# Kernel tuning notes

Measured on AMD Instinct MI355X. Metric: run time of the kernel, lower is better.

Reference implementation:

```python
import jax, jax.numpy as jnp
import numpy as np

B, H, W, C = 16, 56, 56, 512
WS, NH = 7, 16
HD = C // NH
HID = 4 * C
N = WS * WS
NW = (H // WS) * (W // WS)
SCALE = HD ** -0.5
EPS = 1e-5


def _layernorm(x, g, b):
    mu = jnp.mean(x, axis=-1, keepdims=True)
    var = jnp.mean(jnp.square(x - mu), axis=-1, keepdims=True)
    return (x - mu) * jax.lax.rsqrt(var + EPS) * g + b


def _win_part(t):
    # (B,H,W,C) -> (B*nw, NH, N, HD)
    t = t.reshape(B, H // WS, WS, W // WS, WS, C).transpose(0, 1, 3, 2, 4, 5)
    return t.reshape(B * NW, N, NH, HD).transpose(0, 2, 1, 3)


def setup_inputs() -> dict:
    key = jax.random.key(0)
    ks = jax.random.split(key, 20)
    p = lambda k, shp: (jax.random.normal(k, shp, dtype=jnp.float32) * 0.02)
    return {
        "x": jax.random.normal(ks[0], (B, H * W, C), dtype=jnp.float32),
        "Wq": p(ks[1], (C, C)), "bq": jnp.zeros((C,), jnp.float32),
        "Wk": p(ks[2], (C, C)), "bk": jnp.zeros((C,), jnp.float32),
        "Wv": p(ks[3], (C, C)), "bv": jnp.zeros((C,), jnp.float32),
        "Wp": p(ks[4], (C, C)), "bp": jnp.zeros((C,), jnp.float32),
        "rel_bias": p(ks[5], (1, NH, N, N)),
        "g1": jnp.ones((C,), jnp.float32), "b1": jnp.zeros((C,), jnp.float32),
        "g2": jnp.ones((C,), jnp.float32), "b2": jnp.zeros((C,), jnp.float32),
        "W1": p(ks[6], (C, HID)), "bfc1": jnp.zeros((HID,), jnp.float32),
        "W2": p(ks[7], (HID, C)), "bfc2": jnp.zeros((C,), jnp.float32),
    }


def reference(x, Wq, bq, Wk, bk, Wv, bv, Wp, bp, rel_bias,
              g1, b1, g2, b2, W1, bfc1, W2, bfc2):
    shortcut = x                                   # (B, L, C)
    h = _layernorm(x, g1, b1).reshape(B, H, W, C)
    q = _win_part(h @ Wq + bq)                     # (B*nw, NH, N, HD)
    k = _win_part(h @ Wk + bk)
    v = _win_part(h @ Wv + bv)
    attn = jnp.einsum("whnd,whmd->whnm", q * SCALE, k) + rel_bias
    attn = jax.nn.softmax(attn, axis=-1)
    out = jnp.einsum("whnm,whmd->whnd", attn, v)   # (B*nw, NH, N, HD)
    out = out.transpose(0, 2, 1, 3).reshape(B * NW, N, C)
    out = out @ Wp + bp
    # window reverse -> (B, L, C)
    out = out.reshape(B, H // WS, W // WS, WS, WS, C)
    out = out.transpose(0, 1, 3, 2, 4, 5).reshape(B, H * W, C)
    x = shortcut + out
    h2 = _layernorm(x, g2, b2)
    h2 = jax.nn.gelu(h2 @ W1 + bfc1, approximate=False) @ W2 + bfc2
    return x + h2
```

## Files before the change

### kernel.cpp

```cpp
#include <hip/hip_runtime.h>

typedef unsigned short u16;
typedef unsigned int   u32;

using short8  = __attribute__((ext_vector_type(8))) short;
using floatx4 = __attribute__((ext_vector_type(4))) float;

#define Bb   16
#define Hh   56
#define Ww   56
#define Cc   512
#define NHh  16
#define HDd  32
#define HIDh 2048
#define Ll   (Hh*Ww)
#define Mm   (Bb*Ll)
#define SCALE 0.17677669529663687f
#define CSTR 136
#define PSTR 72

__device__ __forceinline__ u16 f2bf(float f) {
  union { float f; u32 u; } v; v.f = f;
  u32 r = (v.u + 0x7fffu + ((v.u >> 16) & 1u)) >> 16;
  return (u16)r;
}
__device__ __forceinline__ float bf2f(u16 u) {
  union { u32 u; float f; } v; v.u = ((u32)u) << 16; return v.f;
}
__device__ __forceinline__ float bf2f_lo(u32 u) {
  union { u32 u; float f; } v; v.u = u << 16; return v.f;
}
__device__ __forceinline__ float bf2f_hi(u32 u) {
  union { u32 u; float f; } v; v.u = u & 0xffff0000u; return v.f;
}
__device__ __forceinline__ float gelu_f(float x) {
  const float z  = x * 0.70710678118654752f;
  const float az = fabsf(z);
  const float t  = __builtin_amdgcn_rcpf(fmaf(0.3275911f, az, 1.f));
  float p = fmaf(1.061405429f, t, -1.453152027f);
  p = fmaf(p, t, 1.421413741f);
  p = fmaf(p, t, -0.284496736f);
  p = fmaf(p, t, 0.254829592f);
  const float e = p * t * __expf(-z * z);
  float erfz = 1.f - e;
  erfz = copysignf(erfz, z);
  return 0.5f * x * (1.f + erfz);
}
__device__ __forceinline__ void gld_lds16(const u16* g, u16* l) {
  __builtin_amdgcn_global_load_lds(
      (__attribute__((address_space(1))) void*)(void*)g,
      (__attribute__((address_space(3))) void*)(void*)l,
      16, 0, 0);
}

__global__ void wcvt_k(const float* __restrict__ W, u16* __restrict__ Wt,
                       int K, int N) {
  int idx = blockIdx.x * 256 + threadIdx.x;
  int n = idx / K;
  int k = idx - n * K;
  Wt[idx] = f2bf(W[(size_t)k * N + n]);
}

__global__ void bcat_k(const float* __restrict__ a, const float* __restrict__ b,
                       const float* __restrict__ c, float* __restrict__ o) {
  int i = blockIdx.x * 256 + threadIdx.x;
  float v = (i < 512) ? a[i] : (i < 1024) ? b[i - 512] : c[i - 1024];
  o[i] = v;
}

__global__ void relprep_k(const float* __restrict__ rel, float* __restrict__ relL) {
  int idx  = blockIdx.x * 256 + threadIdx.x;
  int reg  = idx & 3;
  int lane = (idx >> 2) & 63;
  int frag = (idx >> 8) & 15;
  int h    = idx >> 12;
  int mi = frag >> 2, nj = frag & 3;
  int row = mi * 16 + (lane >> 4) * 4 + reg;
  int col = nj * 16 + (lane & 15);
  float v;
  if (col >= 49)      v = -1e30f;
  else if (row >= 49) v = 0.f;
  else                v = rel[((size_t)h * 49 + row) * 49 + col];
  relL[idx] = v;
}

__global__ __launch_bounds__(256)
void ln_k(const float* __restrict__ x, const float* __restrict__ g,
          const float* __restrict__ b, u16* __restrict__ out) {
  const int row  = blockIdx.x * 4 + (threadIdx.x >> 6);
  const int lane = threadIdx.x & 63;
  const float* xr = x + (size_t)row * Cc + lane * 8;
  float4 v0 = *(const float4*)xr;
  float4 v1 = *(const float4*)(xr + 4);
  float s  = v0.x+v0.y+v0.z+v0.w + v1.x+v1.y+v1.z+v1.w;
  float s2 = v0.x*v0.x+v0.y*v0.y+v0.z*v0.z+v0.w*v0.w
           + v1.x*v1.x+v1.y*v1.y+v1.z*v1.z+v1.w*v1.w;
  #pragma unroll
  for (int off = 32; off >= 1; off >>= 1) {
    s  += __shfl_xor(s,  off);
    s2 += __shfl_xor(s2, off);
  }
  float mu  = s  * (1.f/512.f);
  float var = s2 * (1.f/512.f) - mu*mu;
  float rs  = rsqrtf(var + 1e-5f);
  float4 ga = *(const float4*)(g + lane*8);
  float4 gb = *(const float4*)(g + lane*8 + 4);
  float4 ba = *(const float4*)(b + lane*8);
  float4 bb = *(const float4*)(b + lane*8 + 4);
  float o0 = (v0.x-mu)*rs*ga.x + ba.x;
  float o1 = (v0.y-mu)*rs*ga.y + ba.y;
  float o2 = (v0.z-mu)*rs*ga.z + ba.z;
  float o3 = (v0.w-mu)*rs*ga.w + ba.w;
  float o4 = (v1.x-mu)*rs*gb.x + bb.x;
  float o5 = (v1.y-mu)*rs*gb.y + bb.y;
  float o6 = (v1.z-mu)*rs*gb.z + bb.z;
  float o7 = (v1.w-mu)*rs*gb.w + bb.w;
  u32 w0 = (u32)f2bf(o0) | ((u32)f2bf(o1) << 16);
  u32 w1 = (u32)f2bf(o2) | ((u32)f2bf(o3) << 16);
  u32 w2 = (u32)f2bf(o4) | ((u32)f2bf(o5) << 16);
  u32 w3 = (u32)f2bf(o6) | ((u32)f2bf(o7) << 16);
  *(uint4*)(out + (size_t)row * Cc + lane * 8) = make_uint4(w0, w1, w2, w3);
}

__global__ __launch_bounds__(256)
void ln_bf_k(const u16* __restrict__ x, const float* __restrict__ g,
             const float* __restrict__ b, u16* __restrict__ out) {
  const int row  = blockIdx.x * 4 + (threadIdx.x >> 6);
  const int lane = threadIdx.x & 63;
  uint4 xv = *(const uint4*)(x + (size_t)row * Cc + lane * 8);
  float v[8];
  v[0]=bf2f_lo(xv.x); v[1]=bf2f_hi(xv.x); v[2]=bf2f_lo(xv.y); v[3]=bf2f_hi(xv.y);
  v[4]=bf2f_lo(xv.z); v[5]=bf2f_hi(xv.z); v[6]=bf2f_lo(xv.w); v[7]=bf2f_hi(xv.w);
  float s = 0.f, s2 = 0.f;
  #pragma unroll
  for (int i = 0; i < 8; i++) { s += v[i]; s2 += v[i]*v[i]; }
  #pragma unroll
  for (int off = 32; off >= 1; off >>= 1) {
    s  += __shfl_xor(s,  off);
    s2 += __shfl_xor(s2, off);
  }
  float mu  = s  * (1.f/512.f);
  float var = s2 * (1.f/512.f) - mu*mu;
  float rs  = rsqrtf(var + 1e-5f);
  float4 ga = *(const float4*)(g + lane*8);
  float4 gb = *(const float4*)(g + lane*8 + 4);
  float4 ba = *(const float4*)(b + lane*8);
  float4 bb = *(const float4*)(b + lane*8 + 4);
  float o[8];
  o[0]=(v[0]-mu)*rs*ga.x+ba.x; o[1]=(v[1]-mu)*rs*ga.y+ba.y;
  o[2]=(v[2]-mu)*rs*ga.z+ba.z; o[3]=(v[3]-mu)*rs*ga.w+ba.w;
  o[4]=(v[4]-mu)*rs*gb.x+bb.x; o[5]=(v[5]-mu)*rs*gb.y+bb.y;
  o[6]=(v[6]-mu)*rs*gb.z+bb.z; o[7]=(v[7]-mu)*rs*gb.w+bb.w;
  u32 w0 = (u32)f2bf(o[0]) | ((u32)f2bf(o[1]) << 16);
  u32 w1 = (u32)f2bf(o[2]) | ((u32)f2bf(o[3]) << 16);
  u32 w2 = (u32)f2bf(o[4]) | ((u32)f2bf(o[5]) << 16);
  u32 w3 = (u32)f2bf(o[6]) | ((u32)f2bf(o[7]) << 16);
  *(uint4*)(out + (size_t)row * Cc + lane * 8) = make_uint4(w0, w1, w2, w3);
}

template<int MODE>
__global__ __launch_bounds__(256, 4)
void gemm_bt(const u16* __restrict__ A, const u16* __restrict__ Bt,
             const float* __restrict__ bias, const void* __restrict__ res,
             void* __restrict__ outp, int M, int N, int K, int nbn) {
  (void)M;
  __shared__ __align__(16) u16 smem[128 * CSTR];

  const int b   = blockIdx.x;
  const int xcd = b & 7;
  const int s   = b >> 3;
  const int mt  = (s / nbn) * 8 + xcd;
  const int nt  = s - (s / nbn) * nbn;
  const int m0  = mt * 128;
  const int n0  = nt * 128;

  const int tid  = threadIdx.x;
  const int lane = tid & 63;
  const int wave = tid >> 6;
  const int wm = (wave >> 1) * 64;
  const int wn = (wave & 1) * 64;
  const int quad = lane >> 4;
  const int l16  = lane & 15;

  floatx4 acc[4][4];
  #pragma unroll
  for (int i = 0; i < 4; i++)
    #pragma unroll
    for (int j = 0; j < 4; j++) acc[i][j] = (floatx4)0.f;

  const int r0  = tid >> 2;
  const int cc0 = (((tid & 3) ^ ((r0 >> 1) & 3)) * 8);
  const u16* Ag = A  + (size_t)m0 * K;
  const u16* Bg = Bt + (size_t)n0 * K;

  const int fswz = (l16 >> 1) & 3;
  const int aoff = (quad ^ fswz) * 8;

#define STG(kk, bufo) do {                                                        \
    gld_lds16(Ag + (size_t)r0        * K + (kk) + cc0, &smem[(bufo) + wave * 512]);        \
    gld_lds16(Ag + (size_t)(r0 + 64) * K + (kk) + cc0, &smem[(bufo) + 2048 + wave * 512]); \
    gld_lds16(Bg + (size_t)r0        * K + (kk) + cc0, &smem[(bufo) + 4096 + wave * 512]); \
    gld_lds16(Bg + (size_t)(r0 + 64) * K + (kk) + cc0, &smem[(bufo) + 6144 + wave * 512]); \
  } while (0)

  STG(0, 0);
  asm volatile("s_waitcnt vmcnt(0)" ::: "memory");
  __builtin_amdgcn_s_barrier();

  for (int k0 = 0; k0 < K; k0 += 32) {
    const int bufo = ((k0 >> 5) & 1) * 8192;
    if (k0 + 32 < K) STG(k0 + 32, bufo ^ 8192);
    const u16* As = &smem[bufo];
    const u16* Bs = &smem[bufo + 4096];
    short8 af[4], bf[4];
    #pragma unroll
    for (int mi = 0; mi < 4; mi++)
      af[mi] = *(const short8*)&As[(wm + mi*16 + l16) * 32 + aoff];
    #pragma unroll
    for (int ni = 0; ni < 4; ni++)
      bf[ni] = *(const short8*)&Bs[(wn + ni*16 + l16) * 32 + aoff];
    #pragma unroll
    for (int mi = 0; mi < 4; mi++)
      #pragma unroll
      for (int ni = 0; ni < 4; ni++)
        acc[mi][ni] = __builtin_amdgcn_mfma_f32_16x16x32_bf16(
            af[mi], bf[ni], acc[mi][ni], 0, 0, 0);
    asm volatile("s_waitcnt vmcnt(0)" ::: "memory");
    __builtin_amdgcn_s_barrier();
  }
#undef STG

  if (MODE == 3) {
    const int mrow = m0 + wm + quad * 4;
    const int ncol = n0 + wn + l16;
    #pragma unroll
    for (int ni = 0; ni < 4; ni++) {
      const int n = ncol + ni * 16;
      const float bv = bias[n];
      #pragma unroll
      for (int mi = 0; mi < 4; mi++)
        #pragma unroll
        for (int r = 0; r < 4; r++) {
          const size_t idx = (size_t)(mrow + mi * 16 + r) * N + n;
          ((float*)outp)[idx] = acc[mi][ni][r] + bv + bf2f(((const u16*)res)[idx]);
        }
    }
  } else {
    #pragma unroll
    for (int ni = 0; ni < 4; ni++) {
      const int col = wn + ni * 16 + l16;
      const float bv = bias[n0 + col];
      #pragma unroll
      for (int mi = 0; mi < 4; mi++)
        #pragma unroll
        for (int r = 0; r < 4; r++) {
          float v = acc[mi][ni][r] + bv;
          if (MODE == 1) v = gelu_f(v);
          smem[(wm + mi * 16 + quad * 4 + r) * CSTR + col] = f2bf(v);
        }
    }
    __syncthreads();
    const int trow = tid >> 4;
    const int tcol = (tid & 15) * 8;
    #pragma unroll
    for (int it = 0; it < 8; it++) {
      const int row = it * 16 + trow;
      uint4 w = *(const uint4*)&smem[row * CSTR + tcol];
      const size_t gi = (size_t)(m0 + row) * N + n0 + tcol;
      if (MODE == 2) {
        const float* rp = (const float*)res + gi;
        float4 ra = *(const float4*)rp;
        float4 rb = *(const float4*)(rp + 4);
        u32 w0 = (u32)f2bf(bf2f_lo(w.x) + ra.x) | ((u32)f2bf(bf2f_hi(w.x) + ra.y) << 16);
        u32 w1 = (u32)f2bf(bf2f_lo(w.y) + ra.z) | ((u32)f2bf(bf2f_hi(w.y) + ra.w) << 16);
        u32 w2 = (u32)f2bf(bf2f_lo(w.z) + rb.x) | ((u32)f2bf(bf2f_hi(w.z) + rb.y) << 16);
        u32 w3 = (u32)f2bf(bf2f_lo(w.w) + rb.z) | ((u32)f2bf(bf2f_hi(w.w) + rb.w) << 16);
        *(uint4*)((u16*)outp + gi) = make_uint4(w0, w1, w2, w3);
      } else {
        *(uint4*)((u16*)outp + gi) = w;
      }
    }
  }
}

__global__ __launch_bounds__(256, 3)
void attn_k(const u16* __restrict__ QKV, const float* __restrict__ relL,
            u16* __restrict__ O) {
  __shared__ __align__(16) u16 Vt[4][32][PSTR];
  __shared__ __align__(16) u16 Pl[4][49 * PSTR];

  const int tid  = threadIdx.x;
  const int wave = tid >> 6;
  const int lane = tid & 63;
  const int quad = lane >> 4;
  const int l16  = lane & 15;

  const int win  = blockIdx.x >> 2;
  const int head = ((blockIdx.x & 3) << 2) + wave;
  const int b    = win >> 6;
  const int wh   = (win >> 3) & 7;
  const int ww   = win & 7;
  const int base_l = b * Ll + (wh * 7) * Ww + ww * 7;

  u32 vw[16];
  #pragma unroll
  for (int i = 0; i < 16; i++) vw[i] = 0;
  const int lc = lane < 49 ? lane : 48;
  const size_t grl = (size_t)base_l + (lc / 7) * 56 + (lc % 7);
  if (lane < 49) {
    const uint4* vp = (const uint4*)(QKV + grl * 1536 + 1024 + head * HDd);
    uint4 a0 = vp[0], a1 = vp[1], a2 = vp[2], a3 = vp[3];
    vw[0]=a0.x;  vw[1]=a0.y;  vw[2]=a0.z;  vw[3]=a0.w;
    vw[4]=a1.x;  vw[5]=a1.y;  vw[6]=a1.z;  vw[7]=a1.w;
    vw[8]=a2.x;  vw[9]=a2.y;  vw[10]=a2.z; vw[11]=a2.w;
    vw[12]=a3.x; vw[13]=a3.y; vw[14]=a3.z; vw[15]=a3.w;
  }
  {
    u16* vtb = &Vt[wave][0][lane];
    #pragma unroll
    for (int c = 0; c < 32; c++)
      vtb[c * PSTR] = (u16)(vw[c >> 1] >> ((c & 1) << 4));
  }

  size_t gr16[4];
  #pragma unroll
  for (int t = 0; t < 4; t++) {
    int r = t * 16 + l16; if (r > 48) r = 48;
    gr16[t] = (size_t)base_l + (r / 7) * 56 + (r % 7);
  }
  short8 qf[4], kf[4];
  #pragma unroll
  for (int t = 0; t < 4; t++) {
    qf[t] = *(const short8*)(QKV + gr16[t] * 1536 + head * HDd + quad * 8);
    kf[t] = *(const short8*)(QKV + gr16[t] * 1536 + 512 + head * HDd + quad * 8);
  }

  floatx4 acc[4][4];
  #pragma unroll
  for (int mi = 0; mi < 4; mi++)
    #pragma unroll
    for (int nj = 0; nj < 4; nj++) acc[mi][nj] = (floatx4)0.f;
  #pragma unroll
  for (int mi = 0; mi < 4; mi++)
    #pragma unroll
    for (int nj = 0; nj < 4; nj++)
      acc[mi][nj] = __builtin_amdgcn_mfma_f32_16x16x32_bf16(
          qf[mi], kf[nj], acc[mi][nj], 0, 0, 0);

  const float* rlb = relL + ((size_t)head << 12) + lane * 4;
  #pragma unroll
  for (int mi = 0; mi < 4; mi++)
    #pragma unroll
    for (int nj = 0; nj < 4; nj++) {
      float4 rl = *(const float4*)(rlb + ((mi * 4 + nj) << 8));
      acc[mi][nj][0] = fmaf(acc[mi][nj][0], SCALE, rl.x);
      acc[mi][nj][1] = fmaf(acc[mi][nj][1], SCALE, rl.y);
      acc[mi][nj][2] = fmaf(acc[mi][nj][2], SCALE, rl.z);
      acc[mi][nj][3] = fmaf(acc[mi][nj][3], SCALE, rl.w);
    }

  float sums[4][4];
  #pragma unroll
  for (int mi = 0; mi < 4; mi++)
    #pragma unroll
    for (int r = 0; r < 4; r++) {
      float mx = fmaxf(fmaxf(acc[mi][0][r], acc[mi][1][r]),
                       fmaxf(acc[mi][2][r], acc[mi][3][r]));
      #pragma unroll
      for (int off = 8; off >= 1; off >>= 1)
        mx = fmaxf(mx, __shfl_xor(mx, off));
      float sm = 0.f;
      #pragma unroll
      for (int nj = 0; nj < 4; nj++) {
        float e = __expf(acc[mi][nj][r] - mx);
        acc[mi][nj][r] = e;
        sm += e;
      }
      #pragma unroll
      for (int off = 8; off >= 1; off >>= 1)
        sm += __shfl_xor(sm, off);
      sums[mi][r] = sm;
    }

  u16* Pw = Pl[wave];
  {
    u16* pb = Pw + (quad * 4) * PSTR + l16;
    #pragma unroll
    for (int mi = 0; mi < 3; mi++)
      #pragma unroll
      for (int r = 0; r < 4; r++)
        #pragma unroll
        for (int nj = 0; nj < 4; nj++)
          pb[(mi * 16 + r) * PSTR + nj * 16] = f2bf(acc[mi][nj][r]);
    if (quad == 0) {
      #pragma unroll
      for (int nj = 0; nj < 4; nj++)
        pb[48 * PSTR + nj * 16] = f2bf(acc[3][nj][0]);
    }
  }
  asm volatile("s_waitcnt lgkmcnt(0)" ::: "memory");

  floatx4 pv[4][2];
  #pragma unroll
  for (int mi = 0; mi < 4; mi++)
    #pragma unroll
    for (int nj = 0; nj < 2; nj++) pv[mi][nj] = (floatx4)0.f;
  #pragma unroll
  for (int ks = 0; ks < 2; ks++) {
    short8 pf[4], vf[2];
    #pragma unroll
    for (int mi = 0; mi < 4; mi++) {
      const int pr = (mi < 3) ? (mi * 16 + l16) : 48;
      pf[mi] = *(const short8*)&Pw[pr * PSTR + ks * 32 + quad * 8];
    }
    #pragma unroll
    for (int nj = 0; nj < 2; nj++)
      vf[nj] = *(const short8*)&Vt[wave][nj * 16 + l16][ks * 32 + quad * 8];
    #pragma unroll
    for (int mi = 0; mi < 4; mi++)
      #pragma unroll
      for (int nj = 0; nj < 2; nj++)
        pv[mi][nj] = __builtin_amdgcn_mfma_f32_16x16x32_bf16(
            pf[mi], vf[nj], pv[mi][nj], 0, 0, 0);
  }

  asm volatile("s_waitcnt lgkmcnt(0)" ::: "memory");
  {
    u16* ob = Pw + (quad * 4) * PSTR + l16;
    #pragma unroll
    for (int mi = 0; mi < 3; mi++)
      #pragma unroll
      for (int r = 0; r < 4; r++) {
        const float inv = __builtin_amdgcn_rcpf(sums[mi][r]);
        ob[(mi * 16 + r) * PSTR +  0] = f2bf(pv[mi][0][r] * inv);
        ob[(mi * 16 + r) * PSTR + 16] = f2bf(pv[mi][1][r] * inv);
      }
    if (quad == 0) {
      const float inv = __builtin_amdgcn_rcpf(sums[3][0]);
      ob[48 * PSTR +  0] = f2bf(pv[3][0][0] * inv);
      ob[48 * PSTR + 16] = f2bf(pv[3][1][0] * inv);
    }
  }
  asm volatile("s_waitcnt lgkmcnt(0)" ::: "memory");
  if (lane < 49) {
    const uint4* orow = (const uint4*)&Pw[lane * PSTR];
    uint4* op = (uint4*)(O + grl * 512 + head * HDd);
    op[0] = orow[0]; op[1] = orow[1]; op[2] = orow[2]; op[3] = orow[3];
  }
}

extern "C" void kernel_launch(void* const* d_in, const int* in_sizes, int n_in,
                              void* d_out, int out_size, void* d_ws, size_t ws_size,
                              hipStream_t stream) {
  (void)in_sizes; (void)n_in; (void)out_size; (void)ws_size;
  const float* x    = (const float*)d_in[0];
  const float* Wq   = (const float*)d_in[1];
  const float* bq   = (const float*)d_in[2];
  const float* Wk   = (const float*)d_in[3];
  const float* bk   = (const float*)d_in[4];
  const float* Wv   = (const float*)d_in[5];
  const float* bv   = (const float*)d_in[6];
  const float* Wp   = (const float*)d_in[7];
  const float* bp   = (const float*)d_in[8];
  const float* rel  = (const float*)d_in[9];
  const float* g1   = (const float*)d_in[10];
  const float* b1   = (const float*)d_in[11];
  const float* g2   = (const float*)d_in[12];
  const float* b2   = (const float*)d_in[13];
  const float* W1   = (const float*)d_in[14];
  const float* bfc1 = (const float*)d_in[15];
  const float* W2   = (const float*)d_in[16];
  const float* bfc2 = (const float*)d_in[17];
  float* out = (float*)d_out;

  u16* wQKV = (u16*)d_ws;
  u16* wWp  = wQKV + (size_t)1536*512;
  u16* wW1  = wWp  + (size_t)512*512;
  u16* wW2  = wW1  + (size_t)2048*512;
  float* bqkv = (float*)(wW2 + (size_t)512*2048);
  float* relL = bqkv + 1536;
  u16* hbuf = (u16*)(relL + 65536);
  u16* QKVb = hbuf + (size_t)Mm * Cc;
  u16* Obuf = QKVb + (size_t)Mm * 1536;
  u16* x2bf = Obuf + (size_t)Mm * Cc;
  u16* hid  = QKVb;
  u16* h2   = hbuf;

  wcvt_k<<<(512*512)/256,  256, 0, stream>>>(Wq, wQKV,              512, 512);
  wcvt_k<<<(512*512)/256,  256, 0, stream>>>(Wk, wQKV + 512*512,    512, 512);
  wcvt_k<<<(512*512)/256,  256, 0, stream>>>(Wv, wQKV + 2*512*512,  512, 512);
  wcvt_k<<<(512*512)/256,  256, 0, stream>>>(Wp, wWp, 512, 512);
  wcvt_k<<<(512*2048)/256, 256, 0, stream>>>(W1, wW1, 512, 2048);
  wcvt_k<<<(512*2048)/256, 256, 0, stream>>>(W2, wW2, 2048, 512);
  bcat_k<<<6, 256, 0, stream>>>(bq, bk, bv, bqkv);
  relprep_k<<<65536/256, 256, 0, stream>>>(rel, relL);

  ln_k<<<Mm/4, 256, 0, stream>>>(x, g1, b1, hbuf);

  gemm_bt<0><<<392*12, 256, 0, stream>>>(hbuf, wQKV, bqkv, nullptr, QKVb,
                                         Mm, 1536, 512, 12);

  attn_k<<<4096, 256, 0, stream>>>(QKVb, relL, Obuf);

  gemm_bt<2><<<392*4, 256, 0, stream>>>(Obuf, wWp, bp, x, x2bf,
                                        Mm, 512, 512, 4);

  ln_bf_k<<<Mm/4, 256, 0, stream>>>(x2bf, g2, b2, h2);

  gemm_bt<1><<<392*16, 256, 0, stream>>>(h2, wW1, bfc1, nullptr, hid,
                                         Mm, 2048, 512, 16);
  gemm_bt<3><<<392*4, 256, 0, stream>>>(hid, wW2, bfc2, x2bf, out,
                                        Mm, 512, 2048, 4);
}
```

Measured before the change: 799.1 us.

## Load GEMM fragments directly from global into registers, dropping LDS staging

The bf16 GEMM main loop no longer stages A/B tiles through LDS with global_load_lds and barriers. Each wave now loads its MFMA fragments straight from global memory into registers, double-buffered two k-steps ahead. The occupancy hint is lowered to 3 blocks per SM to make room for the extra registers. This removes LDS traffic and barrier stalls, but the two waves sharing each row or column now each read it from global, so reuse relies on L2/L1 and global traffic goes up.

```diff
diff --git a/kernel.cpp b/kernel.cpp
--- a/kernel.cpp
+++ b/kernel.cpp
@@ -45,12 +45,6 @@
   float erfz = 1.f - e;
   erfz = copysignf(erfz, z);
   return 0.5f * x * (1.f + erfz);
-}
-__device__ __forceinline__ void gld_lds16(const u16* g, u16* l) {
-  __builtin_amdgcn_global_load_lds(
-      (__attribute__((address_space(1))) void*)(void*)g,
-      (__attribute__((address_space(3))) void*)(void*)l,
-      16, 0, 0);
 }
 
 __global__ void wcvt_k(const float* __restrict__ W, u16* __restrict__ Wt,
@@ -159,7 +153,7 @@
 }
 
 template<int MODE>
-__global__ __launch_bounds__(256, 4)
+__global__ __launch_bounds__(256, 3)
 void gemm_bt(const u16* __restrict__ A, const u16* __restrict__ Bt,
              const float* __restrict__ bias, const void* __restrict__ res,
              void* __restrict__ outp, int M, int N, int K, int nbn) {
@@ -188,47 +182,43 @@
     #pragma unroll
     for (int j = 0; j < 4; j++) acc[i][j] = (floatx4)0.f;
 
-  const int r0  = tid >> 2;
-  const int cc0 = (((tid & 3) ^ ((r0 >> 1) & 3)) * 8);
-  const u16* Ag = A  + (size_t)m0 * K;
-  const u16* Bg = Bt + (size_t)n0 * K;
-
-  const int fswz = (l16 >> 1) & 3;
-  const int aoff = (quad ^ fswz) * 8;
-
-#define STG(kk, bufo) do {                                                        \
-    gld_lds16(Ag + (size_t)r0        * K + (kk) + cc0, &smem[(bufo) + wave * 512]);        \
-    gld_lds16(Ag + (size_t)(r0 + 64) * K + (kk) + cc0, &smem[(bufo) + 2048 + wave * 512]); \
-    gld_lds16(Bg + (size_t)r0        * K + (kk) + cc0, &smem[(bufo) + 4096 + wave * 512]); \
-    gld_lds16(Bg + (size_t)(r0 + 64) * K + (kk) + cc0, &smem[(bufo) + 6144 + wave * 512]); \
+  const u16* Ar[4];
+  const u16* Br[4];
+  #pragma unroll
+  for (int i = 0; i < 4; i++) {
+    Ar[i] = A  + (size_t)(m0 + wm + i * 16 + l16) * K + quad * 8;
+    Br[i] = Bt + (size_t)(n0 + wn + i * 16 + l16) * K + quad * 8;
+  }
+
+#define LD(AF, BF, kk) do {                                   \
+    _Pragma("unroll")                                         \
+    for (int i = 0; i < 4; i++) {                             \
+      AF[i] = *(const short8*)(Ar[i] + (kk));                 \
+      BF[i] = *(const short8*)(Br[i] + (kk));                 \
+    }                                                         \
   } while (0)
-
-  STG(0, 0);
-  asm volatile("s_waitcnt vmcnt(0)" ::: "memory");
-  __builtin_amdgcn_s_barrier();
-
-  for (int k0 = 0; k0 < K; k0 += 32) {
-    const int bufo = ((k0 >> 5) & 1) * 8192;
-    if (k0 + 32 < K) STG(k0 + 32, bufo ^ 8192);
-    const u16* As = &smem[bufo];
-    const u16* Bs = &smem[bufo + 4096];
-    short8 af[4], bf[4];
-    #pragma unroll
-    for (int mi = 0; mi < 4; mi++)
-      af[mi] = *(const short8*)&As[(wm + mi*16 + l16) * 32 + aoff];
-    #pragma unroll
-    for (int ni = 0; ni < 4; ni++)
-      bf[ni] = *(const short8*)&Bs[(wn + ni*16 + l16) * 32 + aoff];
-    #pragma unroll
-    for (int mi = 0; mi < 4; mi++)
-      #pragma unroll
-      for (int ni = 0; ni < 4; ni++)
-        acc[mi][ni] = __builtin_amdgcn_mfma_f32_16x16x32_bf16(
-            af[mi], bf[ni], acc[mi][ni], 0, 0, 0);
-    asm volatile("s_waitcnt vmcnt(0)" ::: "memory");
-    __builtin_amdgcn_s_barrier();
-  }
-#undef STG
+#define MM(AF, BF) do {                                       \
+    _Pragma("unroll")                                         \
+    for (int mi = 0; mi < 4; mi++)                            \
+      _Pragma("unroll")                                       \
+      for (int ni = 0; ni < 4; ni++)                          \
+        acc[mi][ni] = __builtin_amdgcn_mfma_f32_16x16x32_bf16(\
+            AF[mi], BF[ni], acc[mi][ni], 0, 0, 0);            \
+  } while (0)
+
+  short8 a0[4], b0[4], a1[4], b1[4];
+  LD(a0, b0, 0);
+  LD(a1, b1, 32);
+  for (int k0 = 0; k0 < K - 64; k0 += 64) {
+    MM(a0, b0);
+    LD(a0, b0, k0 + 64);
+    MM(a1, b1);
+    LD(a1, b1, k0 + 96);
+  }
+  MM(a0, b0);
+  MM(a1, b1);
+#undef LD
+#undef MM
 
   if (MODE == 3) {
     const int mrow = m0 + wm + quad * 4;
```

Result: slower. 1.488 ms (+86.2%).

## Pre-swizzle weights into MFMA fragment order and load B directly to registers

Applied to the files above, without the earlier changes.

The weight conversion kernel now writes the transposed bf16 weights in a layout that matches per-lane MFMA B fragments, so each wave can load its B operands straight from global memory into registers and skip LDS. The GEMM main loop becomes a 4-stage LDS ring for A only, with B register double-buffering, explicit vmcnt waits and sched_barriers that order the loads ahead of the math. The intent is to cut LDS traffic and round trips for B and to overlap loads with MFMA more deeply. In exchange the kernel uses more registers, so launch bounds drop to 3 blocks per CU, and each wave re-reads B from global/L2 without sharing it across waves.

```diff
diff --git a/kernel.cpp b/kernel.cpp
--- a/kernel.cpp
+++ b/kernel.cpp
@@ -56,8 +56,14 @@
 __global__ void wcvt_k(const float* __restrict__ W, u16* __restrict__ Wt,
                        int K, int N) {
   int idx = blockIdx.x * 256 + threadIdx.x;
-  int n = idx / K;
-  int k = idx - n * K;
+  int o    = idx & 7;
+  int lane = (idx >> 3) & 63;
+  int blk  = idx >> 9;
+  int nK32 = K >> 5;
+  int k32  = blk % nK32;
+  int n16  = blk / nK32;
+  int n = n16 * 16 + (lane & 15);
+  int k = k32 * 32 + (lane >> 4) * 8 + o;
   Wt[idx] = f2bf(W[(size_t)k * N + n]);
 }
 
@@ -159,7 +165,7 @@
 }
 
 template<int MODE>
-__global__ __launch_bounds__(256, 4)
+__global__ __launch_bounds__(256, 3)
 void gemm_bt(const u16* __restrict__ A, const u16* __restrict__ Bt,
              const float* __restrict__ bias, const void* __restrict__ res,
              void* __restrict__ outp, int M, int N, int K, int nbn) {
@@ -190,45 +196,92 @@
 
   const int r0  = tid >> 2;
   const int cc0 = (((tid & 3) ^ ((r0 >> 1) & 3)) * 8);
-  const u16* Ag = A  + (size_t)m0 * K;
-  const u16* Bg = Bt + (size_t)n0 * K;
+  const u16* Ag = A + (size_t)m0 * K;
 
   const int fswz = (l16 >> 1) & 3;
   const int aoff = (quad ^ fswz) * 8;
 
-#define STG(kk, bufo) do {                                                        \
-    gld_lds16(Ag + (size_t)r0        * K + (kk) + cc0, &smem[(bufo) + wave * 512]);        \
-    gld_lds16(Ag + (size_t)(r0 + 64) * K + (kk) + cc0, &smem[(bufo) + 2048 + wave * 512]); \
-    gld_lds16(Bg + (size_t)r0        * K + (kk) + cc0, &smem[(bufo) + 4096 + wave * 512]); \
-    gld_lds16(Bg + (size_t)(r0 + 64) * K + (kk) + cc0, &smem[(bufo) + 6144 + wave * 512]); \
+  const int nK32 = K >> 5;
+  const u16* Bf = Bt + (((size_t)((n0 + wn) >> 4) * nK32) << 9) + lane * 8;
+
+#define STGA(t, bufo) do {                                                          \
+    gld_lds16(Ag + (size_t)r0        * K + (t) * 32 + cc0, &smem[(bufo) + wave * 512]);        \
+    gld_lds16(Ag + (size_t)(r0 + 64) * K + (t) * 32 + cc0, &smem[(bufo) + 2048 + wave * 512]); \
   } while (0)
-
-  STG(0, 0);
-  asm volatile("s_waitcnt vmcnt(0)" ::: "memory");
-  __builtin_amdgcn_s_barrier();
-
-  for (int k0 = 0; k0 < K; k0 += 32) {
-    const int bufo = ((k0 >> 5) & 1) * 8192;
-    if (k0 + 32 < K) STG(k0 + 32, bufo ^ 8192);
-    const u16* As = &smem[bufo];
-    const u16* Bs = &smem[bufo + 4096];
-    short8 af[4], bf[4];
-    #pragma unroll
-    for (int mi = 0; mi < 4; mi++)
-      af[mi] = *(const short8*)&As[(wm + mi*16 + l16) * 32 + aoff];
-    #pragma unroll
-    for (int ni = 0; ni < 4; ni++)
-      bf[ni] = *(const short8*)&Bs[(wn + ni*16 + l16) * 32 + aoff];
-    #pragma unroll
-    for (int mi = 0; mi < 4; mi++)
-      #pragma unroll
-      for (int ni = 0; ni < 4; ni++)
-        acc[mi][ni] = __builtin_amdgcn_mfma_f32_16x16x32_bf16(
-            af[mi], bf[ni], acc[mi][ni], 0, 0, 0);
+#define LDB(BF, t) do {                                                             \
+    _Pragma("unroll")                                                               \
+    for (int nj = 0; nj < 4; nj++)                                                  \
+      BF[nj] = *(const short8*)(Bf + (((size_t)nj * nK32 + (t)) << 9));             \
+  } while (0)
+#define DSA(AF, bufo) do {                                                          \
+    _Pragma("unroll")                                                               \
+    for (int mi = 0; mi < 4; mi++)                                                  \
+      AF[mi] = *(const short8*)&smem[(bufo) + (wm + mi * 16 + l16) * 32 + aoff];    \
+  } while (0)
+#define MM(AF, BF) do {                                                             \
+    _Pragma("unroll")                                                               \
+    for (int mi = 0; mi < 4; mi++)                                                  \
+      _Pragma("unroll")                                                             \
+      for (int ni = 0; ni < 4; ni++)                                                \
+        acc[mi][ni] = __builtin_amdgcn_mfma_f32_16x16x32_bf16(                      \
+            AF[mi], BF[ni], acc[mi][ni], 0, 0, 0);                                  \
+  } while (0)
+#define SB() __builtin_amdgcn_sched_barrier(0)
+#define BAR() do { __builtin_amdgcn_s_barrier(); SB(); } while (0)
+#define PHASE(bufC, tS, bufS, BN, tB, BC, CNT) do {                                 \
+    STGA(tS, bufS);                                                                 \
+    SB();                                                                           \
+    LDB(BN, tB);                                                                    \
+    SB();                                                                           \
+    asm volatile("s_waitcnt vmcnt(" CNT ")" ::: "memory");                          \
+    SB();                                                                           \
+    DSA(af, bufC);                                                                  \
+    MM(af, BC);                                                                     \
+    BAR();                                                                          \
+  } while (0)
+
+  const int nT = K >> 5;
+  short8 af[4], b0[4], b1[4];
+
+  STGA(0, 0);
+  SB();
+  STGA(1, 4096);
+  SB();
+  LDB(b0, 0);
+  SB();
+  asm volatile("s_waitcnt vmcnt(6)" ::: "memory");
+  BAR();
+
+  for (int t0 = 0; t0 + 4 < nT; t0 += 4) {
+    PHASE(0,     t0 + 2,  8192, b1, t0 + 1, b0, "6");
+    PHASE(4096,  t0 + 3, 12288, b0, t0 + 2, b1, "6");
+    PHASE(8192,  t0 + 4,     0, b1, t0 + 3, b0, "6");
+    PHASE(12288, t0 + 5,  4096, b0, t0 + 4, b1, "6");
+  }
+  {
+    const int tL = nT - 4;
+    PHASE(0,    tL + 2,  8192, b1, tL + 1, b0, "6");
+    PHASE(4096, tL + 3, 12288, b0, tL + 2, b1, "6");
+    LDB(b1, tL + 3);
+    SB();
+    asm volatile("s_waitcnt vmcnt(4)" ::: "memory");
+    SB();
+    DSA(af, 8192);
+    MM(af, b0);
+    BAR();
     asm volatile("s_waitcnt vmcnt(0)" ::: "memory");
-    __builtin_amdgcn_s_barrier();
-  }
-#undef STG
+    SB();
+    DSA(af, 12288);
+    MM(af, b1);
+    BAR();
+  }
+#undef STGA
+#undef LDB
+#undef DSA
+#undef MM
+#undef SB
+#undef BAR
+#undef PHASE
 
   if (MODE == 3) {
     const int mrow = m0 + wm + quad * 4;
```

Result: faster. 781.3 us (-2.2%).
